# Performance work log

Measured on AMD Instinct MI355X. Metric: run time of the kernel, lower is better.

## Reference

```python
import jax, jax.numpy as jnp
from jax import lax
import numpy as np

B, L, C = 16, 4096, 512
G = 8            # n_groups
CG = C // G      # group_dim = 64
WD = 4           # weather_dim
ORF = 10.0       # offset_range_factor


def conv1d(x, w, b=None):
    # x: [N, Cin, L], w: [Cout, Cin, 3], stride 1, padding 1
    y = lax.conv_general_dilated(x, w, window_strides=(1,), padding=[(1, 1)],
                                 dimension_numbers=('NCH', 'OIH', 'NCH'))
    if b is not None:
        y = y + b[None, :, None]
    return y


def group_norm(x, gamma, beta, groups=4, eps=1e-5):
    N, Cc, Ln = x.shape
    xr = x.reshape(N, groups, Cc // groups, Ln)
    mu = xr.mean(axis=(2, 3), keepdims=True)
    var = ((xr - mu) ** 2).mean(axis=(2, 3), keepdims=True)
    xn = ((xr - mu) / jnp.sqrt(var + eps)).reshape(N, Cc, Ln)
    return xn * gamma[None, :, None] + beta[None, :, None]


def grid_sample_bilinear_border(inp, grid):
    # Faithful torch F.grid_sample(mode='bilinear', padding_mode='border', align_corners=True)
    # inp: [N, C, H, W]; grid: [N, Ho, Wo, 2], grid[...,0]=x (width coord), grid[...,1]=y (height coord)
    N, Cc, H, W = inp.shape
    _, Ho, Wo, _ = grid.shape
    gx, gy = grid[..., 0], grid[..., 1]
    ix = jnp.clip((gx + 1.0) * 0.5 * (W - 1), 0.0, W - 1)  # border padding clamps coords
    iy = jnp.clip((gy + 1.0) * 0.5 * (H - 1), 0.0, H - 1)
    ix0f = jnp.floor(ix); iy0f = jnp.floor(iy)
    wx = ix - ix0f; wy = iy - iy0f
    ix0 = jnp.clip(ix0f.astype(jnp.int32), 0, W - 1)
    iy0 = jnp.clip(iy0f.astype(jnp.int32), 0, H - 1)
    ix1 = jnp.clip(ix0 + 1, 0, W - 1)
    iy1 = jnp.clip(iy0 + 1, 0, H - 1)
    flat = inp.reshape(N, Cc, H * W)
    def gather(iyk, ixk):
        idx = (iyk * W + ixk).reshape(N, 1, Ho * Wo)
        return jnp.take_along_axis(flat, idx, axis=2).reshape(N, Cc, Ho, Wo)
    v00 = gather(iy0, ix0); v01 = gather(iy0, ix1)
    v10 = gather(iy1, ix0); v11 = gather(iy1, ix1)
    wx = wx[:, None, :, :]; wy = wy[:, None, :, :]
    return (v00 * (1 - wy) * (1 - wx) + v01 * (1 - wy) * wx
            + v10 * wy * (1 - wx) + v11 * wy * wx)


def _forward(x, x_ext, w1, b1, gn_g, gn_b, w2, b2, w3, gate):
    xt = jnp.transpose(x, (0, 2, 1))              # [B, C, L]
    xg = xt.reshape(B * G, CG, L)                 # [B*G, CG, L]
    xe = jnp.transpose(x_ext, (0, 2, 1))          # [B, WD, L]
    xe = jnp.tile(xe, (G, 1, 1))                  # torch .repeat(n_groups,1,1)
    pin = jnp.concatenate([xg, xe], axis=1)       # [B*G, CG+WD, L]
    h = jax.nn.gelu(group_norm(conv1d(pin, w1, b1), gn_g, gn_b), approximate=False)
    h = jax.nn.gelu(conv1d(h, w2, b2), approximate=False)
    offset = jnp.tanh(conv1d(h, w3)) * ORF        # [B*G, 1, L]
    off_n = offset * (2.0 / (L - 1.0))
    ref = (jnp.linspace(0.5, L - 0.5, L, dtype=x.dtype) / (L - 1.0)) * 2.0 - 1.0
    grid_x = jnp.clip(ref[None, None, :, None] + off_n[..., None], -1.0, 1.0)  # [B*G,1,L,1]
    grid = jnp.concatenate([grid_x, jnp.zeros_like(grid_x)], axis=-1)
    grid = jnp.transpose(grid, (0, 2, 1, 3))      # [B*G, L, 1, 2]
    xs = grid_sample_bilinear_border(xg[..., None], grid)[..., 0]  # [B*G, CG, L]
    x_out = xg + jnp.tanh(gate) * xs
    x_out = x_out.reshape(B, C, L)
    return jnp.transpose(x_out, (0, 2, 1)), offset


def setup_inputs() -> dict:
    key = jax.random.key(0)
    ks = jax.random.split(key, 8)
    s = 0.05
    return {
        'x': jax.random.normal(ks[0], (B, L, C), jnp.float32),
        'x_ext': jax.random.normal(ks[1], (B, L, WD), jnp.float32),
        'w1': jax.random.normal(ks[2], (64, CG + WD, 3), jnp.float32) * s,
        'b1': jax.random.normal(ks[3], (64,), jnp.float32) * s,
        'gn_g': jnp.ones((64,), jnp.float32),
        'gn_b': jnp.zeros((64,), jnp.float32),
        'w2': jax.random.normal(ks[4], (32, 64, 3), jnp.float32) * s,
        'b2': jax.random.normal(ks[5], (32,), jnp.float32) * s,
        'w3': jax.random.normal(ks[6], (1, 32, 3), jnp.float32) * s,
        'gate': jnp.array([0.5], jnp.float32),
    }


def reference(x, x_ext, w1, b1, gn_g, gn_b, w2, b2, w3, gate):
    return _forward(x, x_ext, w1, b1, gn_g, gn_b, w2, b2, w3, gate)
```

## Files before the change

### kernel.cpp

```cpp
#include <hip/hip_runtime.h>
#include <hip/hip_bf16.h>

#define BB 16
#define LL 4096
#define CC 512
#define NG 128
#define IC1 68
#define OC1 64
#define OC2 32

typedef short short8 __attribute__((ext_vector_type(8)));
typedef float f32x4 __attribute__((ext_vector_type(4)));

__device__ inline ushort f2b(float f) {
    __hip_bfloat16 h = __float2bfloat16(f);
    return *reinterpret_cast<ushort*>(&h);
}
__device__ inline float b2f(ushort u) {
    __hip_bfloat16 h;
    *reinterpret_cast<ushort*>(&h) = u;
    return __bfloat162float(h);
}
__device__ inline float fast_tanh(float y) {
    float e = __expf(2.0f * y);
    return 1.0f - 2.0f / (e + 1.0f);
}
__device__ inline float fast_gelu(float x) {
    float y = x * (0.7978845608f + 0.0356774081f * x * x);
    return 0.5f * x * (1.0f + fast_tanh(y));
}

__global__ __launch_bounds__(256) void k_prep(const float* __restrict__ x,
    const float* __restrict__ w1, const float* __restrict__ w2,
    const float* __restrict__ gate,
    ushort* __restrict__ w1b, ushort* __restrict__ w2b, float* __restrict__ corr)
{
    int idx = blockIdx.x * 256 + threadIdx.x;
    if (idx < 18432) {
        int k = idx / 6144; int r = idx - k * 6144;
        int oc = r / 96;    int icp = r - oc * 96;
        float v = (icp < IC1) ? w1[(oc * IC1 + icp) * 3 + k] : 0.0f;
        w1b[idx] = f2b(v);
    } else if (idx < 24576) {
        int j = idx - 18432;
        int k = j / 2048; int r = j - k * 2048;
        int oc = r / 64;  int ic = r - oc * 64;
        w2b[j] = f2b(w2[(oc * OC1 + ic) * 3 + k]);
    } else if (idx < 32768) {
        int i3 = idx - 24576;
        int b = i3 >> 9; int ch = i3 & 511;
        float tg = tanhf(gate[0]);
        corr[i3] = tg * 0.5f *
            (x[((size_t)(b * LL + 2047)) * CC + ch] +
             x[((size_t)(b * LL + 2048)) * CC + ch]);
    }
}

#define K1_ROWS 130
#define K1_STR  104
__global__ __launch_bounds__(256) void k1_conv1(const float* __restrict__ x,
    const float* __restrict__ xe, const float* __restrict__ b1,
    const ushort* __restrict__ w1b, ushort* __restrict__ h1,
    float* __restrict__ part)
{
    __shared__ ushort pin[K1_ROWS * K1_STR];
    const int n = blockIdx.y, lt = blockIdx.x;
    const int b = n >> 3, g = n & 7, be = n & 15;
    const int l0 = lt * 128;
    const int t = threadIdx.x;

    for (int pos = t; pos < K1_ROWS * 16; pos += 256) {
        int li = pos >> 4, q = pos & 15;
        int l = l0 - 1 + li;
        float4 v = make_float4(0.f, 0.f, 0.f, 0.f);
        if (l >= 0 && l < LL)
            v = *(const float4*)&x[((size_t)(b * LL + l)) * CC + g * 64 + q * 4];
        uint lo = (uint)f2b(v.x) | ((uint)f2b(v.y) << 16);
        uint hi = (uint)f2b(v.z) | ((uint)f2b(v.w) << 16);
        *(uint2*)&pin[li * K1_STR + q * 4] = make_uint2(lo, hi);
    }
    for (int li = t; li < K1_ROWS; li += 256) {
        int l = l0 - 1 + li;
        float4 v = make_float4(0.f, 0.f, 0.f, 0.f);
        if (l >= 0 && l < LL)
            v = *(const float4*)&xe[(size_t)(be * LL + l) * 4];
        uint lo = (uint)f2b(v.x) | ((uint)f2b(v.y) << 16);
        uint hi = (uint)f2b(v.z) | ((uint)f2b(v.w) << 16);
        *(uint2*)&pin[li * K1_STR + 64] = make_uint2(lo, hi);
    }
    {
        uint* pz = (uint*)pin;
        for (int pos = t; pos < K1_ROWS * 14; pos += 256) {
            int li = pos / 14, j = pos - li * 14;
            pz[li * 52 + 34 + j] = 0u;
        }
    }
    __syncthreads();

    const int lane = t & 63;
    const int w = t >> 6;
    const int och = w & 1, lh = w >> 1;
    const int m = lane & 15, h = lane >> 4;

    short8 fa[2][9];
#pragma unroll
    for (int mi = 0; mi < 2; ++mi)
#pragma unroll
        for (int k = 0; k < 3; ++k)
#pragma unroll
            for (int c = 0; c < 3; ++c)
                fa[mi][k * 3 + c] = *(const short8*)&w1b[
                    (size_t)(k * 64 + och * 32 + mi * 16 + m) * 96 + c * 32 + h * 8];

    f32x4 acc[2][4] = {};
#pragma unroll
    for (int tt = 0; tt < 4; ++tt) {
        const int rowbase = lh * 64 + tt * 16 + m;
#pragma unroll
        for (int k = 0; k < 3; ++k) {
#pragma unroll
            for (int c = 0; c < 3; ++c) {
                short8 fb = *(const short8*)&pin[(rowbase + k) * K1_STR + c * 32 + h * 8];
                acc[0][tt] = __builtin_amdgcn_mfma_f32_16x16x32_bf16(fa[0][k * 3 + c], fb, acc[0][tt], 0, 0, 0);
                acc[1][tt] = __builtin_amdgcn_mfma_f32_16x16x32_bf16(fa[1][k * 3 + c], fb, acc[1][tt], 0, 0, 0);
            }
        }
    }

#pragma unroll
    for (int mi = 0; mi < 2; ++mi) {
        float bias[4];
#pragma unroll
        for (int r = 0; r < 4; ++r)
            bias[r] = b1[och * 32 + mi * 16 + h * 4 + r];
        float s1 = 0.f, s2 = 0.f;
#pragma unroll
        for (int tt = 0; tt < 4; ++tt) {
#pragma unroll
            for (int r = 0; r < 4; ++r) {
                float v = acc[mi][tt][r] + bias[r];
                s1 += v; s2 += v * v;
                int oc = och * 32 + mi * 16 + h * 4 + r;
                int l = l0 + lh * 64 + tt * 16 + m;
                h1[((size_t)(n * 64 + oc)) * LL + l] = f2b(v);
            }
        }
#pragma unroll
        for (int off = 32; off > 0; off >>= 1) {
            s1 += __shfl_down(s1, off, 64);
            s2 += __shfl_down(s2, off, 64);
        }
        if (lane == 0) {
            int gidx = och * 2 + mi;
            part[(((size_t)n * 4 + gidx) * 64 + lt * 2 + lh) * 2 + 0] = s1;
            part[(((size_t)n * 4 + gidx) * 64 + lt * 2 + lh) * 2 + 1] = s2;
        }
    }
}

__global__ __launch_bounds__(512) void k2_stats(const float* __restrict__ part,
                                                float* __restrict__ stats)
{
    int tid = threadIdx.x;
    float s1 = 0.f, s2 = 0.f;
    for (int j = 0; j < 64; ++j) {
        s1 += part[((size_t)tid * 64 + j) * 2 + 0];
        s2 += part[((size_t)tid * 64 + j) * 2 + 1];
    }
    float mean = s1 * (1.0f / 65536.0f);
    float var  = s2 * (1.0f / 65536.0f) - mean * mean;
    stats[tid * 2 + 0] = mean;
    stats[tid * 2 + 1] = 1.0f / sqrtf(var + 1e-5f);
}

#define K3_ROWS 130
#define K3_STR  72
#define H2_STR  132
__global__ __launch_bounds__(256) void k3_rest(const ushort* __restrict__ h1,
    const float* __restrict__ stats, const float* __restrict__ gn_g,
    const float* __restrict__ gn_b, const float* __restrict__ b2,
    const ushort* __restrict__ w2b, const float* __restrict__ w3,
    float* __restrict__ offs)
{
    __shared__ ushort p2[K3_ROWS * K3_STR];
    __shared__ float h2s[OC2 * H2_STR];
    const int n = blockIdx.y, lt = blockIdx.x;
    const int l0 = lt * 126;
    const int t = threadIdx.x;

    const int base = (l0 - 2) & ~7;
    for (int pos = t; pos < 64 * 18; pos += 256) {
        int ch = pos / 18, s = pos - ch * 18;
        int ls = base + s * 8;
        ushort u8[8];
        if (ls >= 0 && ls + 8 <= LL) {
            *(uint4*)u8 = *(const uint4*)&h1[((size_t)(n * 64 + ch)) * LL + ls];
        } else {
#pragma unroll
            for (int j = 0; j < 8; ++j) {
                int l = ls + j;
                u8[j] = (l >= 0 && l < LL) ? h1[((size_t)(n * 64 + ch)) * LL + l] : (ushort)0;
            }
        }
        int gi = (n * 4 + (ch >> 4)) * 2;
        float mean = stats[gi], istd = stats[gi + 1];
        float ga = gn_g[ch], bb = gn_b[ch];
#pragma unroll
        for (int j = 0; j < 8; ++j) {
            int l = ls + j;
            int li = l - (l0 - 2);
            if (li < 0 || li >= K3_ROWS) continue;
            float v = 0.f;
            if (l >= 0 && l < LL) {
                float xn = (b2f(u8[j]) - mean) * istd * ga + bb;
                v = fast_gelu(xn);
            }
            p2[li * K3_STR + ch] = f2b(v);
        }
    }
    __syncthreads();

    const int lane = t & 63;
    const int w = t >> 6;
    const int m = lane & 15, h = lane >> 4;

    short8 fa[2][6];
#pragma unroll
    for (int mi = 0; mi < 2; ++mi)
#pragma unroll
        for (int k = 0; k < 3; ++k)
#pragma unroll
            for (int c = 0; c < 2; ++c)
                fa[mi][k * 2 + c] = *(const short8*)&w2b[
                    (size_t)(k * 32 + mi * 16 + m) * 64 + c * 32 + h * 8];

    float bias2[2][4];
#pragma unroll
    for (int mi = 0; mi < 2; ++mi)
#pragma unroll
        for (int r = 0; r < 4; ++r)
            bias2[mi][r] = b2[mi * 16 + h * 4 + r];

    f32x4 acc[2][2] = {};
#pragma unroll
    for (int u = 0; u < 2; ++u) {
        const int jb = (w * 2 + u) * 16 + m;
#pragma unroll
        for (int k = 0; k < 3; ++k) {
#pragma unroll
            for (int c = 0; c < 2; ++c) {
                short8 fb = *(const short8*)&p2[(jb + k) * K3_STR + c * 32 + h * 8];
                acc[0][u] = __builtin_amdgcn_mfma_f32_16x16x32_bf16(fa[0][k * 2 + c], fb, acc[0][u], 0, 0, 0);
                acc[1][u] = __builtin_amdgcn_mfma_f32_16x16x32_bf16(fa[1][k * 2 + c], fb, acc[1][u], 0, 0, 0);
            }
        }
    }
#pragma unroll
    for (int mi = 0; mi < 2; ++mi) {
#pragma unroll
        for (int u = 0; u < 2; ++u) {
            int j = (w * 2 + u) * 16 + m;
            int lj = l0 - 1 + j;
#pragma unroll
            for (int r = 0; r < 4; ++r) {
                int oc = mi * 16 + h * 4 + r;
                float v = 0.f;
                if (lj >= 0 && lj < LL)
                    v = fast_gelu(acc[mi][u][r] + bias2[mi][r]);
                h2s[oc * H2_STR + j] = v;
            }
        }
    }
    __syncthreads();

    for (int q = t; q < 126; q += 256) {
        int l = l0 + q;
        if (l >= LL) break;
        float a = 0.f;
#pragma unroll
        for (int ic = 0; ic < OC2; ++ic) {
            a = fmaf(w3[ic * 3 + 0], h2s[ic * H2_STR + q],     a);
            a = fmaf(w3[ic * 3 + 1], h2s[ic * H2_STR + q + 1], a);
            a = fmaf(w3[ic * 3 + 2], h2s[ic * H2_STR + q + 2], a);
        }
        offs[(size_t)n * LL + l] = fast_tanh(a) * 10.0f;
    }
}

__global__ __launch_bounds__(256) void k0_out(const float* __restrict__ x,
    const float* __restrict__ corr, float* __restrict__ out)
{
    const size_t total4 = (size_t)BB * LL * CC / 4;
    size_t i = (size_t)blockIdx.x * blockDim.x + threadIdx.x;
    size_t stride = (size_t)gridDim.x * blockDim.x;
    for (size_t idx = i; idx < total4; idx += stride) {
        float4 xv = ((const float4*)x)[idx];
        int cidx = (int)((idx >> 19) * 128 + (idx & 127));
        float4 cv = ((const float4*)corr)[cidx];
        float4 o;
        o.x = xv.x + cv.x; o.y = xv.y + cv.y;
        o.z = xv.z + cv.z; o.w = xv.w + cv.w;
        ((float4*)out)[idx] = o;
    }
}

extern "C" void kernel_launch(void* const* d_in, const int* in_sizes, int n_in,
                              void* d_out, int out_size, void* d_ws, size_t ws_size,
                              hipStream_t stream)
{
    const float* x    = (const float*)d_in[0];
    const float* xext = (const float*)d_in[1];
    const float* w1   = (const float*)d_in[2];
    const float* b1   = (const float*)d_in[3];
    const float* gng  = (const float*)d_in[4];
    const float* gnb  = (const float*)d_in[5];
    const float* w2   = (const float*)d_in[6];
    const float* b2   = (const float*)d_in[7];
    const float* w3   = (const float*)d_in[8];
    const float* gate = (const float*)d_in[9];

    float* out  = (float*)d_out;
    float* offs = out + (size_t)BB * LL * CC;

    char* ws = (char*)d_ws;
    ushort* h1  = (ushort*)(ws);
    float* part = (float*)(ws + 67108864);
    float* stats= (float*)(ws + 67371008);
    ushort* w1b = (ushort*)(ws + 67375104);
    ushort* w2b = (ushort*)(ws + 67411968);
    float* corr = (float*)(ws + 67424256);

    k_prep<<<128, 256, 0, stream>>>(x, w1, w2, gate, w1b, w2b, corr);
    dim3 g1(32, NG);
    k1_conv1<<<g1, 256, 0, stream>>>(x, xext, b1, w1b, h1, part);
    k2_stats<<<1, 512, 0, stream>>>(part, stats);
    dim3 g3(33, NG);
    k3_rest<<<g3, 256, 0, stream>>>(h1, stats, gng, gnb, b2, w2b, w3, offs);
    k0_out<<<4096, 256, 0, stream>>>(x, corr, out);
}
```

Measured before the change: 194.5 us.

## Fuse output residual into conv1, fold stats into k3, transpose h1 layout

The elementwise output kernel (x + corr) is folded into the conv1 load loop, so x is read once and out is written while tiles are staged. The single-block stats kernel is removed and each k3 block reduces the partial sums itself. h1 moves from channel-major to position-major layout, so k1 writes and k3 reads become packed vector accesses, and the group-norm affine is precomputed per thread. This drops two launches and a full pass over x, at the cost of redundant stats reductions in every k3 block.

```diff
diff --git a/kernel.cpp b/kernel.cpp
--- a/kernel.cpp
+++ b/kernel.cpp
@@ -60,8 +60,8 @@
 #define K1_STR  104
 __global__ __launch_bounds__(256) void k1_conv1(const float* __restrict__ x,
     const float* __restrict__ xe, const float* __restrict__ b1,
-    const ushort* __restrict__ w1b, ushort* __restrict__ h1,
-    float* __restrict__ part)
+    const ushort* __restrict__ w1b, const float* __restrict__ corr,
+    ushort* __restrict__ h1, float* __restrict__ part, float* __restrict__ out)
 {
     __shared__ ushort pin[K1_ROWS * K1_STR];
     const int n = blockIdx.y, lt = blockIdx.x;
@@ -69,15 +69,26 @@
     const int l0 = lt * 128;
     const int t = threadIdx.x;
 
-    for (int pos = t; pos < K1_ROWS * 16; pos += 256) {
-        int li = pos >> 4, q = pos & 15;
-        int l = l0 - 1 + li;
-        float4 v = make_float4(0.f, 0.f, 0.f, 0.f);
-        if (l >= 0 && l < LL)
-            v = *(const float4*)&x[((size_t)(b * LL + l)) * CC + g * 64 + q * 4];
-        uint lo = (uint)f2b(v.x) | ((uint)f2b(v.y) << 16);
-        uint hi = (uint)f2b(v.z) | ((uint)f2b(v.w) << 16);
-        *(uint2*)&pin[li * K1_STR + q * 4] = make_uint2(lo, hi);
+    {
+        const int q = t & 15;
+        const float4 corrv = *(const float4*)&corr[(b << 9) + g * 64 + q * 4];
+        for (int pos = t; pos < K1_ROWS * 16; pos += 256) {
+            int li = pos >> 4;
+            int l = l0 - 1 + li;
+            float4 v = make_float4(0.f, 0.f, 0.f, 0.f);
+            if (l >= 0 && l < LL) {
+                v = *(const float4*)&x[((size_t)(b * LL + l)) * CC + g * 64 + q * 4];
+                if (li >= 1 && li <= 128) {
+                    float4 o;
+                    o.x = v.x + corrv.x; o.y = v.y + corrv.y;
+                    o.z = v.z + corrv.z; o.w = v.w + corrv.w;
+                    *(float4*)&out[((size_t)(b * LL + l)) * CC + g * 64 + q * 4] = o;
+                }
+            }
+            uint lo = (uint)f2b(v.x) | ((uint)f2b(v.y) << 16);
+            uint hi = (uint)f2b(v.z) | ((uint)f2b(v.w) << 16);
+            *(uint2*)&pin[li * K1_STR + q * 4] = make_uint2(lo, hi);
+        }
     }
     for (int li = t; li < K1_ROWS; li += 256) {
         int l = l0 - 1 + li;
@@ -136,14 +147,17 @@
         float s1 = 0.f, s2 = 0.f;
 #pragma unroll
         for (int tt = 0; tt < 4; ++tt) {
-#pragma unroll
-            for (int r = 0; r < 4; ++r) {
-                float v = acc[mi][tt][r] + bias[r];
-                s1 += v; s2 += v * v;
-                int oc = och * 32 + mi * 16 + h * 4 + r;
-                int l = l0 + lh * 64 + tt * 16 + m;
-                h1[((size_t)(n * 64 + oc)) * LL + l] = f2b(v);
-            }
+            int l = l0 + lh * 64 + tt * 16 + m;
+            float v0 = acc[mi][tt][0] + bias[0];
+            float v1 = acc[mi][tt][1] + bias[1];
+            float v2 = acc[mi][tt][2] + bias[2];
+            float v3 = acc[mi][tt][3] + bias[3];
+            s1 += v0 + v1 + v2 + v3;
+            s2 += v0 * v0 + v1 * v1 + v2 * v2 + v3 * v3;
+            uint2 pk;
+            pk.x = (uint)f2b(v0) | ((uint)f2b(v1) << 16);
+            pk.y = (uint)f2b(v2) | ((uint)f2b(v3) << 16);
+            *(uint2*)&h1[((size_t)n * LL + l) * 64 + och * 32 + mi * 16 + h * 4] = pk;
         }
 #pragma unroll
         for (int off = 32; off > 0; off >>= 1) {
@@ -158,70 +172,76 @@
     }
 }
 
-__global__ __launch_bounds__(512) void k2_stats(const float* __restrict__ part,
-                                                float* __restrict__ stats)
-{
-    int tid = threadIdx.x;
-    float s1 = 0.f, s2 = 0.f;
-    for (int j = 0; j < 64; ++j) {
-        s1 += part[((size_t)tid * 64 + j) * 2 + 0];
-        s2 += part[((size_t)tid * 64 + j) * 2 + 1];
-    }
-    float mean = s1 * (1.0f / 65536.0f);
-    float var  = s2 * (1.0f / 65536.0f) - mean * mean;
-    stats[tid * 2 + 0] = mean;
-    stats[tid * 2 + 1] = 1.0f / sqrtf(var + 1e-5f);
-}
-
 #define K3_ROWS 130
 #define K3_STR  72
 #define H2_STR  132
 __global__ __launch_bounds__(256) void k3_rest(const ushort* __restrict__ h1,
-    const float* __restrict__ stats, const float* __restrict__ gn_g,
+    const float* __restrict__ part, const float* __restrict__ gn_g,
     const float* __restrict__ gn_b, const float* __restrict__ b2,
     const ushort* __restrict__ w2b, const float* __restrict__ w3,
     float* __restrict__ offs)
 {
     __shared__ ushort p2[K3_ROWS * K3_STR];
     __shared__ float h2s[OC2 * H2_STR];
+    __shared__ float sstats[8];
     const int n = blockIdx.y, lt = blockIdx.x;
     const int l0 = lt * 126;
     const int t = threadIdx.x;
-
-    const int base = (l0 - 2) & ~7;
-    for (int pos = t; pos < 64 * 18; pos += 256) {
-        int ch = pos / 18, s = pos - ch * 18;
-        int ls = base + s * 8;
-        ushort u8[8];
-        if (ls >= 0 && ls + 8 <= LL) {
-            *(uint4*)u8 = *(const uint4*)&h1[((size_t)(n * 64 + ch)) * LL + ls];
-        } else {
-#pragma unroll
-            for (int j = 0; j < 8; ++j) {
-                int l = ls + j;
-                u8[j] = (l >= 0 && l < LL) ? h1[((size_t)(n * 64 + ch)) * LL + l] : (ushort)0;
-            }
-        }
-        int gi = (n * 4 + (ch >> 4)) * 2;
-        float mean = stats[gi], istd = stats[gi + 1];
-        float ga = gn_g[ch], bb = gn_b[ch];
-#pragma unroll
-        for (int j = 0; j < 8; ++j) {
-            int l = ls + j;
-            int li = l - (l0 - 2);
-            if (li < 0 || li >= K3_ROWS) continue;
-            float v = 0.f;
-            if (l >= 0 && l < LL) {
-                float xn = (b2f(u8[j]) - mean) * istd * ga + bb;
-                v = fast_gelu(xn);
-            }
-            p2[li * K3_STR + ch] = f2b(v);
-        }
-    }
-    __syncthreads();
-
     const int lane = t & 63;
     const int w = t >> 6;
+
+    {
+        float2 p = *(const float2*)&part[(((size_t)n * 4 + w) * 64 + lane) * 2];
+        float s1 = p.x, s2 = p.y;
+#pragma unroll
+        for (int off = 32; off > 0; off >>= 1) {
+            s1 += __shfl_down(s1, off, 64);
+            s2 += __shfl_down(s2, off, 64);
+        }
+        if (lane == 0) {
+            float mean = s1 * (1.0f / 65536.0f);
+            float var  = s2 * (1.0f / 65536.0f) - mean * mean;
+            sstats[w * 2 + 0] = mean;
+            sstats[w * 2 + 1] = 1.0f / sqrtf(var + 1e-5f);
+        }
+    }
+    __syncthreads();
+
+    const int q = t & 7;
+    float Af[8], Bf[8];
+    {
+        int gi = q >> 1;
+        float mean = sstats[gi * 2], istd = sstats[gi * 2 + 1];
+#pragma unroll
+        for (int j = 0; j < 8; ++j) {
+            float ga = gn_g[q * 8 + j];
+            Af[j] = istd * ga;
+            Bf[j] = gn_b[q * 8 + j] - mean * Af[j];
+        }
+    }
+
+    for (int pos = t; pos < K3_ROWS * 8; pos += 256) {
+        int li = pos >> 3;
+        int l = l0 - 2 + li;
+        uint4 o = make_uint4(0u, 0u, 0u, 0u);
+        if (l >= 0 && l < LL) {
+            uint4 u = *(const uint4*)&h1[((size_t)n * LL + l) * 64 + q * 8];
+            const ushort* us = (const ushort*)&u;
+            ushort vb[8];
+#pragma unroll
+            for (int j = 0; j < 8; ++j) {
+                float xn = fmaf(b2f(us[j]), Af[j], Bf[j]);
+                vb[j] = f2b(fast_gelu(xn));
+            }
+            o.x = (uint)vb[0] | ((uint)vb[1] << 16);
+            o.y = (uint)vb[2] | ((uint)vb[3] << 16);
+            o.z = (uint)vb[4] | ((uint)vb[5] << 16);
+            o.w = (uint)vb[6] | ((uint)vb[7] << 16);
+        }
+        *(uint4*)&p2[li * K3_STR + q * 8] = o;
+    }
+    __syncthreads();
+
     const int m = lane & 15, h = lane >> 4;
 
     short8 fa[2][6];
@@ -273,34 +293,17 @@
     }
     __syncthreads();
 
-    for (int q = t; q < 126; q += 256) {
-        int l = l0 + q;
+    for (int qq = t; qq < 126; qq += 256) {
+        int l = l0 + qq;
         if (l >= LL) break;
         float a = 0.f;
 #pragma unroll
         for (int ic = 0; ic < OC2; ++ic) {
-            a = fmaf(w3[ic * 3 + 0], h2s[ic * H2_STR + q],     a);
-            a = fmaf(w3[ic * 3 + 1], h2s[ic * H2_STR + q + 1], a);
-            a = fmaf(w3[ic * 3 + 2], h2s[ic * H2_STR + q + 2], a);
+            a = fmaf(w3[ic * 3 + 0], h2s[ic * H2_STR + qq],     a);
+            a = fmaf(w3[ic * 3 + 1], h2s[ic * H2_STR + qq + 1], a);
+            a = fmaf(w3[ic * 3 + 2], h2s[ic * H2_STR + qq + 2], a);
         }
         offs[(size_t)n * LL + l] = fast_tanh(a) * 10.0f;
-    }
-}
-
-__global__ __launch_bounds__(256) void k0_out(const float* __restrict__ x,
-    const float* __restrict__ corr, float* __restrict__ out)
-{
-    const size_t total4 = (size_t)BB * LL * CC / 4;
-    size_t i = (size_t)blockIdx.x * blockDim.x + threadIdx.x;
-    size_t stride = (size_t)gridDim.x * blockDim.x;
-    for (size_t idx = i; idx < total4; idx += stride) {
-        float4 xv = ((const float4*)x)[idx];
-        int cidx = (int)((idx >> 19) * 128 + (idx & 127));
-        float4 cv = ((const float4*)corr)[cidx];
-        float4 o;
-        o.x = xv.x + cv.x; o.y = xv.y + cv.y;
-        o.z = xv.z + cv.z; o.w = xv.w + cv.w;
-        ((float4*)out)[idx] = o;
     }
 }
 
@@ -325,16 +328,13 @@
     char* ws = (char*)d_ws;
     ushort* h1  = (ushort*)(ws);
     float* part = (float*)(ws + 67108864);
-    float* stats= (float*)(ws + 67371008);
-    ushort* w1b = (ushort*)(ws + 67375104);
-    ushort* w2b = (ushort*)(ws + 67411968);
-    float* corr = (float*)(ws + 67424256);
+    ushort* w1b = (ushort*)(ws + 67371008);
+    ushort* w2b = (ushort*)(ws + 67407872);
+    float* corr = (float*)(ws + 67420160);
 
     k_prep<<<128, 256, 0, stream>>>(x, w1, w2, gate, w1b, w2b, corr);
     dim3 g1(32, NG);
-    k1_conv1<<<g1, 256, 0, stream>>>(x, xext, b1, w1b, h1, part);
-    k2_stats<<<1, 512, 0, stream>>>(part, stats);
+    k1_conv1<<<g1, 256, 0, stream>>>(x, xext, b1, w1b, corr, h1, part, out);
     dim3 g3(33, NG);
-    k3_rest<<<g3, 256, 0, stream>>>(h1, stats, gng, gnb, b2, w2b, w3, offs);
-    k0_out<<<4096, 256, 0, stream>>>(x, corr, out);
-}
+    k3_rest<<<g3, 256, 0, stream>>>(h1, part, gng, gnb, b2, w2b, w3, offs);
+}
```

New measurement: 156.1 us. 1.25x faster.
